# Optimization experiments

Hardware: AMD Instinct MI355X
Metric: run time of the kernel (lower is better)

Reference implementation:

```python
import jax, jax.numpy as jnp
import numpy as np

B, T, D = 2, 2048, 2048
H, HD = 32, 64  # n_heads, head_dim; H*HD == attn_dim == D


def _rope(x, cos, sin):
    # x: (B,T,H,HD) with interleaved (real, imag) pairs on last dim
    b, t, h, hd = x.shape
    x2 = x.reshape(b, t, h, hd // 2, 2)
    xr, xi = x2[..., 0], x2[..., 1]
    c = cos[None, :, None, :]  # (1,T,1,HD/2)
    s = sin[None, :, None, :]
    out_r = xr * c - xi * s
    out_i = xr * s + xi * c
    return jnp.stack([out_r, out_i], axis=-1).reshape(b, t, h, hd)


def setup_inputs() -> dict:
    key = jax.random.key(0)
    ks = jax.random.split(key, 5)
    x = jax.random.normal(ks[0], (B, T, D), dtype=jnp.float32)
    scale = 0.02
    wq = jax.random.normal(ks[1], (D, D), dtype=jnp.float32) * scale
    wk = jax.random.normal(ks[2], (D, D), dtype=jnp.float32) * scale
    wv = jax.random.normal(ks[3], (D, D), dtype=jnp.float32) * scale
    wo = jax.random.normal(ks[4], (D, D), dtype=jnp.float32) * scale
    # standard RoPE frequencies, theta = 10000
    inv_freq = 1.0 / (10000.0 ** (jnp.arange(0, HD, 2, dtype=jnp.float32) / HD))  # (HD/2,)
    angles = jnp.arange(T, dtype=jnp.float32)[:, None] * inv_freq[None, :]  # (T, HD/2)
    return {
        "x": x,
        "freqs_cos": jnp.cos(angles),
        "freqs_sin": jnp.sin(angles),
        "wq": wq, "wk": wk, "wv": wv, "wo": wo,
    }


def reference(x, freqs_cos, freqs_sin, wq, wk, wv, wo):
    b, t, d = x.shape
    # fused-style QKV projections (nn.Linear: x @ W.T, no bias)
    q = (x @ wq.T).reshape(b, t, H, HD)
    k = (x @ wk.T).reshape(b, t, H, HD)
    v = (x @ wv.T).reshape(b, t, H, HD)
    q = _rope(q, freqs_cos, freqs_sin)
    k = _rope(k, freqs_cos, freqs_sin)
    # causal SDPA, scale = 1/sqrt(head_dim)
    scale = 1.0 / jnp.sqrt(jnp.float32(HD))
    scores = jnp.einsum("bqhd,bkhd->bhqk", q, k) * scale  # (B,H,T,T)
    causal = jnp.tril(jnp.ones((t, t), dtype=bool))
    scores = jnp.where(causal[None, None], scores, jnp.float32(-jnp.inf))
    attn = jax.nn.softmax(scores, axis=-1)
    y = jnp.einsum("bhqk,bkhd->bqhd", attn, v).reshape(b, t, H * HD)
    return y @ wo.T
```

## Files before the change

kernel.cpp:

```cpp
#include <hip/hip_runtime.h>
#include <hip/hip_bf16.h>
#include <stdint.h>


typedef __bf16 bf16_t;
typedef __bf16 bf16x4 __attribute__((ext_vector_type(4)));
typedef __bf16 bf16x8 __attribute__((ext_vector_type(8)));
typedef float  f32x4  __attribute__((ext_vector_type(4)));

constexpr int B_ = 2, T_ = 2048, D_ = 2048, H_ = 32, HD_ = 64;
constexpr int M_ = B_ * T_;

__device__ __forceinline__ void async_copy16(const bf16_t* g, bf16_t* l) {
  __builtin_amdgcn_global_load_lds(
      (const __attribute__((address_space(1))) void*)g,
      (__attribute__((address_space(3))) void*)l, 16, 0, 0);
}

__global__ __launch_bounds__(256) void cast_f32_bf16(
    const float* __restrict__ src, bf16_t* __restrict__ dst, int n4)
{
  const int i = blockIdx.x * 256 + threadIdx.x;
  if (i >= n4) return;
  const float4 v = ((const float4*)src)[i];
  bf16x4 o;
  o[0] = (bf16_t)v.x; o[1] = (bf16_t)v.y; o[2] = (bf16_t)v.z; o[3] = (bf16_t)v.w;
  ((bf16x4*)dst)[i] = o;
}

__global__ __launch_bounds__(256) void cast_qkvx(
    const float* __restrict__ x, const float* __restrict__ wq,
    const float* __restrict__ wk, const float* __restrict__ wv,
    bf16_t* __restrict__ xb, bf16_t* __restrict__ wb3, int nx4, int nw4)
{
  const int i = blockIdx.x * 256 + threadIdx.x;
  const int total = nx4 + 3 * nw4;
  if (i >= total) return;
  const float* src; bf16_t* dst; int idx;
  if (i < nx4) { src = x; dst = xb; idx = i; }
  else {
    const int j = i - nx4;
    const int wsel = j / nw4;
    idx = j - wsel * nw4;
    src = (wsel == 0) ? wq : (wsel == 1) ? wk : wv;
    dst = wb3 + (size_t)wsel * (size_t)nw4 * 4;
  }
  const float4 v = ((const float4*)src)[idx];
  bf16x4 o;
  o[0] = (bf16_t)v.x; o[1] = (bf16_t)v.y; o[2] = (bf16_t)v.z; o[3] = (bf16_t)v.w;
  ((bf16x4*)dst)[idx] = o;
}

template <typename OutT>
__global__ __launch_bounds__(256, 2) void gemm_bt(
    const bf16_t* __restrict__ A, const bf16_t* __restrict__ B,
    OutT* __restrict__ C, int M, int N, int K)
{
  __shared__ __attribute__((aligned(16))) bf16_t As[128 * 32];
  __shared__ __attribute__((aligned(16))) bf16_t Bs[128 * 32];

  const int tid    = threadIdx.x;
  const int w      = tid >> 6;
  const int l      = tid & 63;
  const int quad   = l >> 4;
  const int lane16 = l & 15;
  const int bm0 = blockIdx.x * 128;
  const int bn0 = blockIdx.y * 128;
  const int wm  = (w >> 1) * 64;
  const int wn  = (w & 1) * 64;
  const int srow = l >> 2;
  const int scol = (l & 3) * 8;

  const bf16_t* Ag = A + (size_t)bm0 * K;
  const bf16_t* Bg = B + (size_t)bn0 * K;

  f32x4 acc[4][4] = {};

  for (int kk = 0; kk < K; kk += 32) {
    __syncthreads();
#pragma unroll
    for (int s0 = 0; s0 < 2; ++s0) {
      const int s = w + s0 * 4;
      async_copy16(Ag + (size_t)(s * 16 + srow) * K + kk + scol, &As[s * 512]);
      async_copy16(Bg + (size_t)(s * 16 + srow) * K + kk + scol, &Bs[s * 512]);
    }
    __syncthreads();

    bf16x8 af[4], bfr[4];
#pragma unroll
    for (int i = 0; i < 4; ++i)
      af[i] = *(const bf16x8*)&As[(wm + i * 16 + lane16) * 32 + quad * 8];
#pragma unroll
    for (int j = 0; j < 4; ++j)
      bfr[j] = *(const bf16x8*)&Bs[(wn + j * 16 + lane16) * 32 + quad * 8];
#pragma unroll
    for (int i = 0; i < 4; ++i)
#pragma unroll
      for (int j = 0; j < 4; ++j)
        acc[i][j] = __builtin_amdgcn_mfma_f32_16x16x32_bf16(af[i], bfr[j],
                                                            acc[i][j], 0, 0, 0);
  }

#pragma unroll
  for (int i = 0; i < 4; ++i) {
#pragma unroll
    for (int r = 0; r < 4; ++r) {
      const size_t row = (size_t)(bm0 + wm + i * 16 + quad * 4 + r);
#pragma unroll
      for (int j = 0; j < 4; ++j) {
        const int col = bn0 + wn + j * 16 + lane16;
        C[row * N + col] = (OutT)acc[i][j][r];
      }
    }
  }
}

__global__ __launch_bounds__(256, 2) void gemm_qkv(
    const bf16_t* __restrict__ A, const bf16_t* __restrict__ B,
    bf16_t* __restrict__ Cq, bf16_t* __restrict__ Ck, bf16_t* __restrict__ Cv,
    const float* __restrict__ fc, const float* __restrict__ fs,
    int M, int K)
{
  __shared__ __attribute__((aligned(16))) bf16_t As[128 * 32];
  __shared__ __attribute__((aligned(16))) bf16_t Bs[128 * 32];

  const int tid    = threadIdx.x;
  const int w      = tid >> 6;
  const int l      = tid & 63;
  const int quad   = l >> 4;
  const int lane16 = l & 15;
  const int bm0 = blockIdx.x * 128;
  const int bn0 = blockIdx.y * 128;
  const int wm  = (w >> 1) * 64;
  const int wn  = (w & 1) * 64;
  const int srow = l >> 2;
  const int scol = (l & 3) * 8;

  const bf16_t* Ag = A + (size_t)bm0 * K;
  const bf16_t* Bg = B + (size_t)bn0 * K;

  f32x4 acc[4][4] = {};

  for (int kk = 0; kk < K; kk += 32) {
    __syncthreads();
#pragma unroll
    for (int s0 = 0; s0 < 2; ++s0) {
      const int s = w + s0 * 4;
      async_copy16(Ag + (size_t)(s * 16 + srow) * K + kk + scol, &As[s * 512]);
      async_copy16(Bg + (size_t)(s * 16 + srow) * K + kk + scol, &Bs[s * 512]);
    }
    __syncthreads();

    bf16x8 af[4], bfr[4];
#pragma unroll
    for (int i = 0; i < 4; ++i)
      af[i] = *(const bf16x8*)&As[(wm + i * 16 + lane16) * 32 + quad * 8];
#pragma unroll
    for (int j = 0; j < 4; ++j)
      bfr[j] = *(const bf16x8*)&Bs[(wn + j * 16 + lane16) * 32 + quad * 8];
#pragma unroll
    for (int i = 0; i < 4; ++i)
#pragma unroll
      for (int j = 0; j < 4; ++j)
        acc[i][j] = __builtin_amdgcn_mfma_f32_16x16x32_bf16(af[i], bfr[j],
                                                            acc[i][j], 0, 0, 0);
  }

  bf16_t* Cb; float qs; int dorope;
  if (bn0 < 2048)      { Cb = Cq; qs = 0.125f; dorope = 1; }
  else if (bn0 < 4096) { Cb = Ck; qs = 1.0f;   dorope = 1; }
  else                 { Cb = Cv; qs = 1.0f;   dorope = 0; }
  const int cb0 = (bn0 & 2047) + wn;
#pragma unroll
  for (int i = 0; i < 4; ++i) {
#pragma unroll
    for (int r = 0; r < 4; ++r) {
      const size_t row = (size_t)(bm0 + wm + i * 16 + quad * 4 + r);
      const int t = (int)(row & (T_ - 1));
#pragma unroll
      for (int j = 0; j < 4; ++j) {
        float v = acc[i][j][r];
        if (dorope) {
          const int hd = j * 16 + lane16;
          const float c  = fc[t * 32 + (hd >> 1)];
          const float s  = fs[t * 32 + (hd >> 1)];
          const float pr = __shfl_xor(v, 1);
          v = ((hd & 1) ? (pr * s + v * c) : (v * c - pr * s)) * qs;
        }
        Cb[row * 2048 + cb0 + j * 16 + lane16] = (bf16_t)v;
      }
    }
  }
}

__global__ __launch_bounds__(256) void rope_kernel(
    bf16_t* __restrict__ q, bf16_t* __restrict__ k,
    const float* __restrict__ cosb, const float* __restrict__ sinb, int npair)
{
  const int idx = blockIdx.x * 256 + threadIdx.x;
  if (idx >= npair) return;
  const int p = idx & 31;
  const int t = (idx >> 10) & (T_ - 1);
  const float c = cosb[t * 32 + p];
  const float s = sinb[t * 32 + p];
  const size_t off = (size_t)idx * 2;

  const float qr = (float)q[off], qi = (float)q[off + 1];
  q[off]     = (bf16_t)((qr * c - qi * s) * 0.125f);
  q[off + 1] = (bf16_t)((qr * s + qi * c) * 0.125f);

  const float kr = (float)k[off], ki = (float)k[off + 1];
  k[off]     = (bf16_t)(kr * c - ki * s);
  k[off + 1] = (bf16_t)(kr * s + ki * c);
}

__global__ __launch_bounds__(256, 2) void flash_attn(
    const bf16_t* __restrict__ Q, const bf16_t* __restrict__ K,
    const bf16_t* __restrict__ V, bf16_t* __restrict__ Y)
{
  __shared__ __attribute__((aligned(16))) bf16_t Vf[4096];
  __shared__ __attribute__((aligned(16))) bf16_t Pt[4 * 2 * 16 * 68];

  const int tid    = threadIdx.x;
  const int w      = tid >> 6;
  const int l      = tid & 63;
  const int quad   = l >> 4;
  const int lane16 = l & 15;
  const int bh = blockIdx.y;
  const int b  = bh >> 5;
  const int h  = bh & 31;
  const int gx = blockIdx.x;
  int qa[2];
  qa[0] = gx * 128 + w * 32;
  qa[1] = (15 - gx) * 128 + w * 32;
  const size_t rs = (size_t)H_ * HD_;

  const bf16_t* Qb = Q + ((size_t)b * T_) * rs + h * HD_;
  const bf16_t* Kb = K + ((size_t)b * T_) * rs + h * HD_;
  const bf16_t* Vb = V + ((size_t)b * T_) * rs + h * HD_;

  bf16x8 qf[2][2][2];
#pragma unroll
  for (int g = 0; g < 2; ++g)
#pragma unroll
    for (int t = 0; t < 2; ++t)
#pragma unroll
      for (int c = 0; c < 2; ++c)
        qf[g][t][c] = *(const bf16x8*)(Qb + (size_t)(qa[g] + t * 16 + lane16) * rs +
                                       c * 32 + quad * 8);

  f32x4 o[2][2][4] = {};
  float lsum[2][2] = {};

  const int koff = tid >> 3;
  const int oct  = tid & 7;
  const int d0   = oct * 8;
  const int nV = oct >> 1, base16 = (oct & 1) * 8;

  bf16_t* const PtW = Pt + w * (2 * 16 * 68);

  const int nsteps = (15 - gx) * 2 + 2;

  bf16x8 vr[2];
#pragma unroll
  for (int hf = 0; hf < 2; ++hf)
    vr[hf] = *(const bf16x8*)(Vb + (size_t)(hf * 32 + koff) * rs + d0);

  for (int it = 0; it < nsteps; ++it) {
    const int k0 = it * 64;
    __syncthreads();
#pragma unroll
    for (int hf = 0; hf < 2; ++hf) {
      const int key = hf * 32 + koff;
      const int cV = key >> 5, qV = (key >> 3) & 3, jV = key & 7;
#pragma unroll
      for (int i = 0; i < 8; ++i) {
        const int gv = ((cV * 4 + nV) * 16 + base16 + i) * 4 + qV;
        Vf[(gv ^ oct) * 8 + jV] = vr[hf][i];
      }
    }
    __syncthreads();
    if (it + 1 < nsteps) {
      const int k0n = k0 + 64;
#pragma unroll
      for (int hf = 0; hf < 2; ++hf)
        vr[hf] = *(const bf16x8*)(Vb + (size_t)(k0n + hf * 32 + koff) * rs + d0);
    }

    bf16x8 kf2[2][4];
#pragma unroll
    for (int c = 0; c < 2; ++c)
#pragma unroll
      for (int kt = 0; kt < 4; ++kt)
        kf2[c][kt] = *(const bf16x8*)(Kb + (size_t)(k0 + kt * 16 + lane16) * rs +
                                      c * 32 + quad * 8);

#pragma unroll
    for (int g = 0; g < 2; ++g) {
      if (k0 > qa[g] + 31) continue;

      f32x4 stx[4][2] = {};
#pragma unroll
      for (int c = 0; c < 2; ++c) {
#pragma unroll
        for (int kt = 0; kt < 4; ++kt) {
          stx[kt][0] = __builtin_amdgcn_mfma_f32_16x16x32_bf16(kf2[c][kt], qf[g][0][c],
                                                               stx[kt][0], 0, 0, 0);
          stx[kt][1] = __builtin_amdgcn_mfma_f32_16x16x32_bf16(kf2[c][kt], qf[g][1][c],
                                                               stx[kt][1], 0, 0, 0);
        }
      }

#pragma unroll
      for (int t = 0; t < 2; ++t) {
        const int qbase = qa[g] + t * 16;
#pragma unroll
        for (int kt = 0; kt < 4; ++kt) {
          const int kbase = k0 + kt * 16 + quad * 4;
          const bool anymask = (k0 + kt * 16 + 15) > qbase;
          float p[4];
#pragma unroll
          for (int r = 0; r < 4; ++r) {
            float s = stx[kt][t][r];
            if (anymask) s = (kbase + r > qbase + lane16) ? -1e30f : s;
            p[r] = __expf(s);
          }
          lsum[g][t] += (p[0] + p[1]) + (p[2] + p[3]);
          bf16x4 pv;
          pv[0] = (bf16_t)p[0]; pv[1] = (bf16_t)p[1];
          pv[2] = (bf16_t)p[2]; pv[3] = (bf16_t)p[3];
          *(bf16x4*)&PtW[(t * 16 + lane16) * 68 + kt * 16 + quad * 4] = pv;
        }
      }

#pragma unroll
      for (int c = 0; c < 2; ++c) {
        const bf16x8 pf0 = *(const bf16x8*)&PtW[(0 * 16 + lane16) * 68 + c * 32 + quad * 8];
        const bf16x8 pf1 = *(const bf16x8*)&PtW[(1 * 16 + lane16) * 68 + c * 32 + quad * 8];
#pragma unroll
        for (int n = 0; n < 4; ++n) {
          const int gv = ((c * 4 + n) * 16 + lane16) * 4 + quad;
          const int swz = n * 2 + (lane16 >> 3);
          const bf16x8 vfr = *(const bf16x8*)&Vf[(gv ^ swz) * 8];
          o[g][0][n] = __builtin_amdgcn_mfma_f32_16x16x32_bf16(pf0, vfr, o[g][0][n], 0, 0, 0);
          o[g][1][n] = __builtin_amdgcn_mfma_f32_16x16x32_bf16(pf1, vfr, o[g][1][n], 0, 0, 0);
        }
      }
    }
  }

  bf16_t* Yb = Y + ((size_t)b * T_) * rs + h * HD_;
#pragma unroll
  for (int g = 0; g < 2; ++g) {
#pragma unroll
    for (int t = 0; t < 2; ++t) {
      float lt = lsum[g][t];
      lt += __shfl_xor(lt, 16);
      lt += __shfl_xor(lt, 32);
#pragma unroll
      for (int r = 0; r < 4; ++r) {
        const float linv = 1.0f / __shfl(lt, quad * 4 + r);
        const size_t row = (size_t)(qa[g] + t * 16 + quad * 4 + r);
#pragma unroll
        for (int n = 0; n < 4; ++n)
          Yb[row * rs + n * 16 + lane16] = (bf16_t)(o[g][t][n][r] * linv);
      }
    }
  }
}

extern "C" void kernel_launch(void* const* d_in, const int* in_sizes, int n_in,
                              void* d_out, int out_size, void* d_ws, size_t ws_size,
                              hipStream_t stream)
{
  (void)in_sizes; (void)n_in; (void)out_size;
  const float* x  = (const float*)d_in[0];
  const float* fc = (const float*)d_in[1];
  const float* fs = (const float*)d_in[2];
  const float* wq = (const float*)d_in[3];
  const float* wk = (const float*)d_in[4];
  const float* wv = (const float*)d_in[5];
  const float* wo = (const float*)d_in[6];
  float* out = (float*)d_out;

  const size_t nx = (size_t)M_ * D_;
  const size_t nw = (size_t)D_ * D_;
  const dim3 blk(256);
  const int nx4 = (int)(nx / 4), nw4 = (int)(nw / 4);
  const dim3 gg(M_ / 128, D_ / 128);

  if (ws_size >= (3 * nw + 4 * nx) * sizeof(bf16_t)) {
    bf16_t* ws  = (bf16_t*)d_ws;
    bf16_t* wb3 = ws;
    bf16_t* xb  = ws + 3 * nw;
    bf16_t* qb  = xb + nx;
    bf16_t* kb  = qb + nx;
    bf16_t* vb  = kb + nx;
    bf16_t* yb  = xb;

    const int ntot4 = nx4 + 3 * nw4;
    cast_qkvx<<<dim3(ntot4 / 256), blk, 0, stream>>>(x, wq, wk, wv, xb, wb3,
                                                     nx4, nw4);

    gemm_qkv<<<dim3(M_ / 128, 48), blk, 0, stream>>>(xb, wb3, qb, kb, vb,
                                                     fc, fs, M_, D_);

    flash_attn<<<dim3(8, B_ * H_), blk, 0, stream>>>(qb, kb, vb, yb);

    cast_f32_bf16<<<dim3(nw4 / 256), blk, 0, stream>>>(wo, wb3, nw4);
    gemm_bt<float><<<gg, blk, 0, stream>>>(yb, wb3, out, M_, D_, D_);
  } else {
    bf16_t* ws = (bf16_t*)d_ws;
    bf16_t* wb = ws;
    bf16_t* xb = ws + nw;
    bf16_t* qb = xb + nx;
    bf16_t* kb = qb + nx;
    bf16_t* vb = kb + nx;
    bf16_t* yb = xb;

    cast_f32_bf16<<<dim3(nx4 / 256), blk, 0, stream>>>(x, xb, nx4);
    cast_f32_bf16<<<dim3(nw4 / 256), blk, 0, stream>>>(wq, wb, nw4);
    gemm_bt<bf16_t><<<gg, blk, 0, stream>>>(xb, wb, qb, M_, D_, D_);
    cast_f32_bf16<<<dim3(nw4 / 256), blk, 0, stream>>>(wk, wb, nw4);
    gemm_bt<bf16_t><<<gg, blk, 0, stream>>>(xb, wb, kb, M_, D_, D_);
    cast_f32_bf16<<<dim3(nw4 / 256), blk, 0, stream>>>(wv, wb, nw4);
    gemm_bt<bf16_t><<<gg, blk, 0, stream>>>(xb, wb, vb, M_, D_, D_);

    rope_kernel<<<dim3((B_ * T_ * H_ * 32) / 256), blk, 0, stream>>>(
        qb, kb, fc, fs, B_ * T_ * H_ * 32);
    flash_attn<<<dim3(8, B_ * H_), blk, 0, stream>>>(qb, kb, vb, yb);

    cast_f32_bf16<<<dim3(nw4 / 256), blk, 0, stream>>>(wo, wb, nw4);
    gemm_bt<float><<<gg, blk, 0, stream>>>(yb, wb, out, M_, D_, D_);
  }
}
```

Measured before the change: 416.2 us.

## Rewrite QKV GEMM as 8-wave 128x256 tile with triple-buffered LDS pipeline

Replaces the QKV projection GEMM with a 512-thread kernel computing 128x256 tiles over 64-wide K steps. It uses a three-stage async global-to-LDS ring, XOR-swizzled LDS layout against bank conflicts, and interleaves loads with MFMA phases under s_setprio. Blocks are remapped for cache locality. The aim is to hide global memory latency and raise MFMA utilisation, at the cost of higher LDS use (144KB), one block per CU and a manual vmcnt/barrier schedule that is fragile.

```diff
diff --git a/kernel.cpp b/kernel.cpp
--- a/kernel.cpp
+++ b/kernel.cpp
@@ -16,6 +16,9 @@
       (const __attribute__((address_space(1))) void*)g,
       (__attribute__((address_space(3))) void*)l, 16, 0, 0);
 }
+
+#define GQ_BAR()   __builtin_amdgcn_s_barrier()
+#define GQ_FENCE() asm volatile("" ::: "memory")
 
 __global__ __launch_bounds__(256) void cast_f32_bf16(
     const float* __restrict__ src, bf16_t* __restrict__ dst, int n4)
@@ -115,56 +118,153 @@
   }
 }
 
-__global__ __launch_bounds__(256, 2) void gemm_qkv(
-    const bf16_t* __restrict__ A, const bf16_t* __restrict__ B,
+__global__ __launch_bounds__(512, 1) void gemm_qkv8(
+    const bf16_t* __restrict__ A, const bf16_t* __restrict__ Bw,
     bf16_t* __restrict__ Cq, bf16_t* __restrict__ Ck, bf16_t* __restrict__ Cv,
-    const float* __restrict__ fc, const float* __restrict__ fs,
-    int M, int K)
-{
-  __shared__ __attribute__((aligned(16))) bf16_t As[128 * 32];
-  __shared__ __attribute__((aligned(16))) bf16_t Bs[128 * 32];
+    const float* __restrict__ fc, const float* __restrict__ fs)
+{
+  __shared__ __attribute__((aligned(16))) bf16_t lds[3 * 24576];
+  constexpr int K = 2048;
+  constexpr int NT = 32;
 
   const int tid    = threadIdx.x;
   const int w      = tid >> 6;
   const int l      = tid & 63;
   const int quad   = l >> 4;
   const int lane16 = l & 15;
-  const int bm0 = blockIdx.x * 128;
-  const int bn0 = blockIdx.y * 128;
-  const int wm  = (w >> 1) * 64;
-  const int wn  = (w & 1) * 64;
-  const int srow = l >> 2;
-  const int scol = (l & 3) * 8;
-
-  const bf16_t* Ag = A + (size_t)bm0 * K;
-  const bf16_t* Bg = B + (size_t)bn0 * K;
+  const int wm = (w >> 2) * 64;
+  const int wn = (w & 3) * 64;
+
+  const int lin = (blockIdx.x & 7) * 96 + (blockIdx.x >> 3);
+  const int bm0 = (lin & 31) << 7;
+  const int bn0 = (lin >> 5) << 8;
+
+  const int rsel = (tid >> 3) & 7;
+  const size_t soff = (size_t)(tid >> 3) * K + (((tid & 7) ^ rsel) << 3);
+
+  const bf16_t* Ag = A  + (size_t)bm0 * K;
+  const bf16_t* Bg = Bw + (size_t)bn0 * K;
+
+  auto stS = [&](const bf16_t* gb, int s, int kt, int ebase) {
+    async_copy16(gb + (size_t)(s * 64) * K + kt * 64 + soff,
+                 &lds[ebase + s * 4096 + w * 512]);
+  };
+
+  const int r7  = lane16 & 7;
+  const int sw0 = ((0 + quad) ^ r7) << 4;
+  const int sw1 = ((4 + quad) ^ r7) << 4;
+  const char* ldsc = (const char*)lds;
 
   f32x4 acc[4][4] = {};
 
-  for (int kk = 0; kk < K; kk += 32) {
-    __syncthreads();
-#pragma unroll
-    for (int s0 = 0; s0 < 2; ++s0) {
-      const int s = w + s0 * 4;
-      async_copy16(Ag + (size_t)(s * 16 + srow) * K + kk + scol, &As[s * 512]);
-      async_copy16(Bg + (size_t)(s * 16 + srow) * K + kk + scol, &Bs[s * 512]);
-    }
-    __syncthreads();
-
-    bf16x8 af[4], bfr[4];
-#pragma unroll
-    for (int i = 0; i < 4; ++i)
-      af[i] = *(const bf16x8*)&As[(wm + i * 16 + lane16) * 32 + quad * 8];
-#pragma unroll
-    for (int j = 0; j < 4; ++j)
-      bfr[j] = *(const bf16x8*)&Bs[(wn + j * 16 + lane16) * 32 + quad * 8];
-#pragma unroll
-    for (int i = 0; i < 4; ++i)
-#pragma unroll
-      for (int j = 0; j < 4; ++j)
-        acc[i][j] = __builtin_amdgcn_mfma_f32_16x16x32_bf16(af[i], bfr[j],
-                                                            acc[i][j], 0, 0, 0);
-  }
+#pragma unroll
+  for (int s = 0; s < 4; ++s) stS(Bg, s, 0, 0 * 24576 + 8192);
+#pragma unroll
+  for (int s = 0; s < 2; ++s) stS(Ag, s, 0, 0 * 24576);
+#pragma unroll
+  for (int s = 0; s < 4; ++s) stS(Bg, s, 1, 1 * 24576 + 8192);
+#pragma unroll
+  for (int s = 0; s < 2; ++s) stS(Ag, s, 1, 1 * 24576);
+  asm volatile("s_waitcnt vmcnt(6)" ::: "memory");
+  GQ_BAR();
+  GQ_FENCE();
+
+  int cur = 0, stg = 2;
+#pragma unroll 1
+  for (int t = 0; t < NT; ++t) {
+    const int ktn = (t + 2 < NT) ? t + 2 : NT - 1;
+    const int cb = cur * 49152;
+    const int sA = stg * 24576;
+    const int sB = sA + 8192;
+
+    bf16x8 a0[2][2], a1[2][2], b0[2][2], b1[2][2];
+
+#pragma unroll
+    for (int i = 0; i < 2; ++i) {
+      const int ra = (wm + i * 16 + lane16) * 128;
+      a0[i][0] = *(const bf16x8*)(ldsc + cb + ra + sw0);
+      a0[i][1] = *(const bf16x8*)(ldsc + cb + ra + sw1);
+    }
+#pragma unroll
+    for (int j = 0; j < 2; ++j) {
+      const int rb = (wn + j * 16 + lane16) * 128;
+      b0[j][0] = *(const bf16x8*)(ldsc + cb + 16384 + rb + sw0);
+      b0[j][1] = *(const bf16x8*)(ldsc + cb + 16384 + rb + sw1);
+    }
+    stS(Bg, 0, ktn, sB); stS(Bg, 1, ktn, sB);
+    GQ_BAR(); GQ_FENCE();
+    __builtin_amdgcn_s_setprio(1);
+#pragma unroll
+    for (int i = 0; i < 2; ++i)
+#pragma unroll
+      for (int j = 0; j < 2; ++j)
+#pragma unroll
+        for (int ks = 0; ks < 2; ++ks)
+          acc[i][j] = __builtin_amdgcn_mfma_f32_16x16x32_bf16(
+              a0[i][ks], b0[j][ks], acc[i][j], 0, 0, 0);
+    __builtin_amdgcn_s_setprio(0);
+    GQ_BAR(); GQ_FENCE();
+
+#pragma unroll
+    for (int i = 0; i < 2; ++i) {
+      const int ra = (wm + 32 + i * 16 + lane16) * 128;
+      a1[i][0] = *(const bf16x8*)(ldsc + cb + ra + sw0);
+      a1[i][1] = *(const bf16x8*)(ldsc + cb + ra + sw1);
+    }
+    stS(Bg, 2, ktn, sB); stS(Bg, 3, ktn, sB);
+    GQ_BAR(); GQ_FENCE();
+    __builtin_amdgcn_s_setprio(1);
+#pragma unroll
+    for (int i = 0; i < 2; ++i)
+#pragma unroll
+      for (int j = 0; j < 2; ++j)
+#pragma unroll
+        for (int ks = 0; ks < 2; ++ks)
+          acc[2 + i][j] = __builtin_amdgcn_mfma_f32_16x16x32_bf16(
+              a1[i][ks], b0[j][ks], acc[2 + i][j], 0, 0, 0);
+    __builtin_amdgcn_s_setprio(0);
+    GQ_BAR(); GQ_FENCE();
+
+#pragma unroll
+    for (int j = 0; j < 2; ++j) {
+      const int rb = (wn + 32 + j * 16 + lane16) * 128;
+      b1[j][0] = *(const bf16x8*)(ldsc + cb + 16384 + rb + sw0);
+      b1[j][1] = *(const bf16x8*)(ldsc + cb + 16384 + rb + sw1);
+    }
+    stS(Ag, 0, ktn, sA);
+    GQ_BAR(); GQ_FENCE();
+    __builtin_amdgcn_s_setprio(1);
+#pragma unroll
+    for (int i = 0; i < 2; ++i)
+#pragma unroll
+      for (int j = 0; j < 2; ++j)
+#pragma unroll
+        for (int ks = 0; ks < 2; ++ks)
+          acc[i][2 + j] = __builtin_amdgcn_mfma_f32_16x16x32_bf16(
+              a0[i][ks], b1[j][ks], acc[i][2 + j], 0, 0, 0);
+    __builtin_amdgcn_s_setprio(0);
+    GQ_BAR(); GQ_FENCE();
+
+    stS(Ag, 1, ktn, sA);
+    GQ_BAR(); GQ_FENCE();
+    __builtin_amdgcn_s_setprio(1);
+#pragma unroll
+    for (int i = 0; i < 2; ++i)
+#pragma unroll
+      for (int j = 0; j < 2; ++j)
+#pragma unroll
+        for (int ks = 0; ks < 2; ++ks)
+          acc[2 + i][2 + j] = __builtin_amdgcn_mfma_f32_16x16x32_bf16(
+              a1[i][ks], b1[j][ks], acc[2 + i][2 + j], 0, 0, 0);
+    __builtin_amdgcn_s_setprio(0);
+    asm volatile("s_waitcnt vmcnt(6)" ::: "memory");
+    GQ_BAR(); GQ_FENCE();
+
+    cur = (cur == 2) ? 0 : cur + 1;
+    stg = (stg == 2) ? 0 : stg + 1;
+  }
+
+  asm volatile("s_waitcnt vmcnt(0)" ::: "memory");
 
   bf16_t* Cb; float qs; int dorope;
   if (bn0 < 2048)      { Cb = Cq; qs = 0.125f; dorope = 1; }
@@ -402,8 +502,7 @@
     cast_qkvx<<<dim3(ntot4 / 256), blk, 0, stream>>>(x, wq, wk, wv, xb, wb3,
                                                      nx4, nw4);
 
-    gemm_qkv<<<dim3(M_ / 128, 48), blk, 0, stream>>>(xb, wb3, qb, kb, vb,
-                                                     fc, fs, M_, D_);
+    gemm_qkv8<<<dim3(768), dim3(512), 0, stream>>>(xb, wb3, qb, kb, vb, fc, fs);
 
     flash_attn<<<dim3(8, B_ * H_), blk, 0, stream>>>(qb, kb, vb, yb);
 
```

New measurement: 415.5 us. Within noise of the previous version (-0.2%).
